# Optimization experiments

Measured on AMD Instinct MI355X. Metric: run time of the kernel, lower is better.

## Reference

```python
import jax, jax.numpy as jnp
import numpy as np

T, B, I, H, O = 1024, 64, 256, 512, 5

def setup_inputs() -> dict:
    key = jax.random.key(0)
    ks = jax.random.split(key, 7)
    s_ih = 1.0 / np.sqrt(H)
    return {
        "inputs": jax.random.normal(ks[0], (T, B, I), dtype=jnp.float32),
        "W_ih": jax.random.uniform(ks[1], (4 * H, I), minval=-s_ih, maxval=s_ih, dtype=jnp.float32),
        "W_hh": jax.random.uniform(ks[2], (4 * H, H), minval=-s_ih, maxval=s_ih, dtype=jnp.float32),
        "b_ih": jax.random.uniform(ks[3], (4 * H,), minval=-s_ih, maxval=s_ih, dtype=jnp.float32),
        "b_hh": jax.random.uniform(ks[4], (4 * H,), minval=-s_ih, maxval=s_ih, dtype=jnp.float32),
        "fc_w": jax.random.uniform(ks[5], (O, H), minval=-s_ih, maxval=s_ih, dtype=jnp.float32),
        "fc_b": jax.random.uniform(ks[6], (O,), minval=-s_ih, maxval=s_ih, dtype=jnp.float32),
    }

def _lstm_step(carry, x_t, W_ih, W_hh, b_ih, b_hh):
    h, c = carry
    # gates: [B, 4H]
    gates = x_t @ W_ih.T + b_ih + h @ W_hh.T + b_hh
    i_g, f_g, g_g, o_g = jnp.split(gates, 4, axis=-1)
    i_g = jax.nn.sigmoid(i_g)
    f_g = jax.nn.sigmoid(f_g)
    g_g = jnp.tanh(g_g)
    o_g = jax.nn.sigmoid(o_g)
    c_new = f_g * c + i_g * g_g
    h_new = o_g * jnp.tanh(c_new)
    return (h_new, c_new), h_new

def reference(inputs, W_ih, W_hh, b_ih, b_hh, fc_w, fc_b):
    batch = inputs.shape[1]
    h0 = jnp.zeros((batch, H), dtype=inputs.dtype)
    c0 = jnp.zeros((batch, H), dtype=inputs.dtype)
    step = lambda carry, x_t: _lstm_step(carry, x_t, W_ih, W_hh, b_ih, b_hh)
    (h_T, c_T), hs = jax.lax.scan(step, (h0, c0), inputs)  # hs: [T, B, H]
    outputs = hs @ fc_w.T + fc_b  # [T, B, O]
    return outputs, (h_T, c_T)
```

## Files before the change

### kernel.cpp

```cpp
#include <hip/hip_runtime.h>
#include <stdint.h>

#define T_ 1024
#define B_ 64
#define I_ 256
#define H_ 512
#define O_ 5
#define NCHAIN 8
#define NB 8
#define JW 16
#define GRID_MAIN 256
#define BLOCK_MAIN 256
#define XBS 264
#define EX_OFF 4096
#define BH (B_*H_)
#define TBO (T_*B_*O_)
#define POISON 0x7F7F7F7Fu

typedef __bf16 bf16x8 __attribute__((ext_vector_type(8)));
typedef float floatx4 __attribute__((ext_vector_type(4)));
typedef unsigned short u16;
typedef unsigned short u16x8 __attribute__((ext_vector_type(8)));
typedef unsigned int u32;
typedef u32 u32x4 __attribute__((ext_vector_type(4)));

__device__ __forceinline__ u16 f2bf(float f) {
  unsigned int u = __float_as_uint(f);
  u += 0x7fffu + ((u >> 16) & 1u);
  return (u16)(u >> 16);
}
__device__ __forceinline__ float bf2f(u16 v) {
  return __uint_as_float(((unsigned int)v) << 16);
}
__device__ __forceinline__ float sigmoid_f(float x) {
  return 1.0f / (1.0f + __expf(-x));
}
__device__ __forceinline__ float tanh_f(float x) {
  return 2.0f / (1.0f + __expf(-2.0f * x)) - 1.0f;
}

__device__ __forceinline__ void store_u32_l3(u32* p, u32 v) {
  asm volatile("global_store_dword %0, %1, off sc0 sc1" :: "v"(p), "v"(v) : "memory");
}

__device__ __forceinline__ void load_h4_l3(const u16* p, u32x4* r) {
  asm volatile(
    "global_load_dwordx4 %0, %4, off sc0 sc1\n\t"
    "global_load_dwordx4 %1, %4, off offset:64 sc0 sc1\n\t"
    "global_load_dwordx4 %2, %4, off offset:128 sc0 sc1\n\t"
    "global_load_dwordx4 %3, %4, off offset:192 sc0 sc1\n\t"
    "s_waitcnt vmcnt(0)"
    : "=&v"(r[0]), "=&v"(r[1]), "=&v"(r[2]), "=&v"(r[3]) : "v"(p) : "memory");
}
__device__ __forceinline__ void load_h6_l3(const u16* p, u32x4* r) {
  asm volatile(
    "global_load_dwordx4 %0, %6, off sc0 sc1\n\t"
    "global_load_dwordx4 %1, %6, off offset:64 sc0 sc1\n\t"
    "global_load_dwordx4 %2, %6, off offset:128 sc0 sc1\n\t"
    "global_load_dwordx4 %3, %6, off offset:192 sc0 sc1\n\t"
    "global_load_dwordx4 %4, %6, off offset:256 sc0 sc1\n\t"
    "global_load_dwordx4 %5, %6, off offset:320 sc0 sc1\n\t"
    "s_waitcnt vmcnt(0)"
    : "=&v"(r[0]), "=&v"(r[1]), "=&v"(r[2]), "=&v"(r[3]), "=&v"(r[4]), "=&v"(r[5])
    : "v"(p) : "memory");
}

__device__ __forceinline__ void barrier_lds() {
  asm volatile("s_waitcnt lgkmcnt(0)\n\ts_barrier" ::: "memory");
}

__device__ __forceinline__ void stage_x(const float* __restrict__ xsrc,
                                        u16 (*xb)[XBS], int u) {
  #pragma unroll
  for (int i = 0; i < 2; ++i) {
    int cid = u + 128 * i;
    int b  = cid >> 5;
    int ko = (cid & 31) * 8;
    const float4* s = (const float4*)(xsrc + (size_t)b * I_ + ko);
    float4 f0 = s[0], f1 = s[1];
    u16x8 uu;
    uu[0]=f2bf(f0.x); uu[1]=f2bf(f0.y); uu[2]=f2bf(f0.z); uu[3]=f2bf(f0.w);
    uu[4]=f2bf(f1.x); uu[5]=f2bf(f1.y); uu[6]=f2bf(f1.z); uu[7]=f2bf(f1.w);
    *(u16x8*)&xb[b][ko] = uu;
  }
}

__global__ __launch_bounds__(BLOCK_MAIN, 1)
void lstm_persistent(const float* __restrict__ x,
                     const float* __restrict__ W_ih,
                     const float* __restrict__ W_hh,
                     const float* __restrict__ b_ih,
                     const float* __restrict__ b_hh,
                     float* __restrict__ out,
                     u16* __restrict__ hist)
{
  __shared__ __align__(16) u16 xbuf[2][NB][XBS];
  __shared__ float part[4 * 4 * 16 * 17];

  const int tid  = threadIdx.x;
  const int wg   = blockIdx.x;
  const int w    = tid >> 6;
  const int lane = tid & 63;
  const int q    = lane >> 4;
  const int n    = lane & 15;
  const int chain = wg & 7;
  const int jslot = wg >> 3;
  const int jbase = jslot * JW;
  const int bbase = chain * NB;

  bf16x8 afrag[4][6];
  #pragma unroll
  for (int g = 0; g < 4; ++g) {
    #pragma unroll
    for (int kk = 0; kk < 6; ++kk) {
      const int kc  = w * 6 + kk;
      const int row = g * H_ + jbase + n;
      const float* src;
      if (kc < 8) src = W_ih + (size_t)row * I_ + kc * 32 + q * 8;
      else        src = W_hh + (size_t)row * H_ + (kc - 8) * 32 + q * 8;
      float4 f0 = ((const float4*)src)[0];
      float4 f1 = ((const float4*)src)[1];
      bf16x8 a;
      a[0]=(__bf16)f0.x; a[1]=(__bf16)f0.y; a[2]=(__bf16)f0.z; a[3]=(__bf16)f0.w;
      a[4]=(__bf16)f1.x; a[5]=(__bf16)f1.y; a[6]=(__bf16)f1.z; a[7]=(__bf16)f1.w;
      afrag[g][kk] = a;
    }
  }

  const int eb = tid >> 4;
  const int ej = tid & 15;
  float bias[4];
  float cval = 0.0f;
  if (tid < 128) {
    #pragma unroll
    for (int g = 0; g < 4; ++g)
      bias[g] = b_ih[g * H_ + jbase + ej] + b_hh[g * H_ + jbase + ej];
  }

  const int nx   = (w == 0) ? 6 : ((w == 1) ? 2 : 0);
  const int hoff = (w == 2) ? 128 : ((w == 3) ? 320 : 0);

  if (tid >= 128) stage_x(x + (size_t)bbase * I_, xbuf[0], tid - 128);
  __syncthreads();

  for (int t = 0; t < T_; ++t) {
    const int sr = t & 1, sw = (t + 1) & 1;

    bf16x8 bfrag[6];
    #pragma unroll
    for (int kk = 0; kk < 6; ++kk)
      if (kk < nx)
        bfrag[kk] = __builtin_bit_cast(bf16x8,
            *(const uint4*)&xbuf[sr][n & 7][(w * 6 + kk) * 32 + q * 8]);

    if (w > 0) {
      const u16* hp = hist + (size_t)t * BH + (size_t)(bbase + (n & 7)) * H_ +
                      hoff + q * 8;
      if (w == 1) {
        u32x4 r[4];
        for (;;) {
          load_h4_l3(hp, r);
          u32 bad = 0;
          #pragma unroll
          for (int i = 0; i < 4; ++i)
            #pragma unroll
            for (int jj = 0; jj < 4; ++jj) bad |= (r[i][jj] == POISON);
          if (!__any((int)bad)) break;
        }
        #pragma unroll
        for (int i = 0; i < 4; ++i)
          bfrag[2 + i] = __builtin_bit_cast(bf16x8, r[i]);
      } else {
        u32x4 r[6];
        for (;;) {
          load_h6_l3(hp, r);
          u32 bad = 0;
          #pragma unroll
          for (int i = 0; i < 6; ++i)
            #pragma unroll
            for (int jj = 0; jj < 4; ++jj) bad |= (r[i][jj] == POISON);
          if (!__any((int)bad)) break;
        }
        #pragma unroll
        for (int i = 0; i < 6; ++i)
          bfrag[i] = __builtin_bit_cast(bf16x8, r[i]);
      }
    }

    floatx4 acc[4] = {};
    #pragma unroll
    for (int kk = 0; kk < 6; ++kk) {
      #pragma unroll
      for (int g = 0; g < 4; ++g)
        acc[g] = __builtin_amdgcn_mfma_f32_16x16x32_bf16(afrag[g][kk], bfrag[kk], acc[g], 0, 0, 0);
    }

    #pragma unroll
    for (int g = 0; g < 4; ++g)
      #pragma unroll
      for (int r = 0; r < 4; ++r)
        part[((w * 4 + g) * 16 + (q * 4 + r)) * 17 + n] = acc[g][r];
    barrier_lds();

    if (tid < 128) {
      float gate[4];
      #pragma unroll
      for (int g = 0; g < 4; ++g) {
        float s = bias[g];
        #pragma unroll
        for (int w2 = 0; w2 < 4; ++w2)
          s += part[((w2 * 4 + g) * 16 + ej) * 17 + eb];
        gate[g] = s;
      }
      const float ig = sigmoid_f(gate[0]);
      const float fg = sigmoid_f(gate[1]);
      const float gg = tanh_f(gate[2]);
      const float og = sigmoid_f(gate[3]);
      cval = fg * cval + ig * gg;
      const float hval = og * tanh_f(cval);
      const int bg = bbase + eb;
      const int jg = jbase + ej;
      const u32 hb = (u32)f2bf(hval);
      const u32 other = __shfl_xor((int)hb, 1, 64);
      if ((tid & 1) == 0) {
        const u32 packed = hb | (other << 16);
        store_u32_l3((u32*)(hist + (size_t)(t + 1) * BH + (size_t)bg * H_ + jg), packed);
      }
      if (t == T_ - 1) {
        out[TBO + (size_t)bg * H_ + jg]      = hval;
        out[TBO + BH + (size_t)bg * H_ + jg] = cval;
      }
    } else {
      const int ts = (t + 1 < T_) ? (t + 1) : (T_ - 1);
      stage_x(x + ((size_t)ts * B_ + bbase) * I_, xbuf[sw], tid - 128);
    }
    barrier_lds();
  }
}

__global__ __launch_bounds__(256)
void fc_kernel(const u16* __restrict__ hist,
               const float* __restrict__ fc_w,
               const float* __restrict__ fc_b,
               float* __restrict__ out)
{
  const int gw   = (blockIdx.x * 256 + threadIdx.x) >> 6;
  const int lane = threadIdx.x & 63;
  const int t = gw >> 6;
  const int b = gw & 63;
  const u16* hrow = hist + ((size_t)(t + 1) * B_ + b) * H_ + lane * 8;
  uint4 hv = *(const uint4*)hrow;
  float h[8];
  {
    u16x8 hu = __builtin_bit_cast(u16x8, hv);
    #pragma unroll
    for (int i = 0; i < 8; ++i) h[i] = bf2f(hu[i]);
  }
  float accs[O_];
  #pragma unroll
  for (int o = 0; o < O_; ++o) {
    const float* wr = fc_w + (size_t)o * H_ + lane * 8;
    float4 w0 = ((const float4*)wr)[0];
    float4 w1 = ((const float4*)wr)[1];
    accs[o] = h[0]*w0.x + h[1]*w0.y + h[2]*w0.z + h[3]*w0.w
            + h[4]*w1.x + h[5]*w1.y + h[6]*w1.z + h[7]*w1.w;
  }
  #pragma unroll
  for (int o = 0; o < O_; ++o)
    #pragma unroll
    for (int off = 32; off > 0; off >>= 1)
      accs[o] += __shfl_down(accs[o], off, 64);
  if (lane == 0) {
    #pragma unroll
    for (int o = 0; o < O_; ++o)
      out[((size_t)t * B_ + b) * O_ + o] = accs[o] + fc_b[o];
  }
}

extern "C" void kernel_launch(void* const* d_in, const int* in_sizes, int n_in,
                              void* d_out, int out_size, void* d_ws, size_t ws_size,
                              hipStream_t stream)
{
  (void)in_sizes; (void)n_in; (void)out_size; (void)ws_size;
  const float* x    = (const float*)d_in[0];
  const float* W_ih = (const float*)d_in[1];
  const float* W_hh = (const float*)d_in[2];
  const float* b_ih = (const float*)d_in[3];
  const float* b_hh = (const float*)d_in[4];
  const float* fc_w = (const float*)d_in[5];
  const float* fc_b = (const float*)d_in[6];
  float* out = (float*)d_out;

  u16* hist = (u16*)((char*)d_ws + EX_OFF);

  hipMemsetAsync(d_ws, 0, EX_OFF + (size_t)BH * 2, stream);
  hipMemsetAsync((char*)d_ws + EX_OFF + (size_t)BH * 2, 0x7F,
                 (size_t)T_ * BH * 2, stream);

  lstm_persistent<<<GRID_MAIN, BLOCK_MAIN, 0, stream>>>(
      x, W_ih, W_hh, b_ih, b_hh, out, hist);
  fc_kernel<<<(T_ * B_) / 4, 256, 0, stream>>>(hist, fc_w, fc_b, out);
}
```

Measured before the change: 2.103 ms.

## Use XCD-local L2 polling for hidden state and drop the trailing barrier

At startup each workgroup reads its XCC id and publishes it, and each chain checks whether all of its workgroups sit on the same XCD. If they do, the h-history polling loads use L2-coherent (sc0) loads instead of system-scope loads, with a periodic fallback to the full-coherence load, and h stores are written both plainly and with sc0 sc1. The partial-sum LDS buffer is double-buffered so the trailing per-step barrier can be removed, and x staging moves to the start of the step. The aim is lower cross-workgroup sync latency per timestep. The risks are stale L2 data if the XCD assumption fails, and LDS hazards from removing the barrier.

Result: slower. 5.434 ms (+158.4%).

```diff
diff --git a/kernel.cpp b/kernel.cpp
--- a/kernel.cpp
+++ b/kernel.cpp
@@ -6,12 +6,12 @@
 #define I_ 256
 #define H_ 512
 #define O_ 5
-#define NCHAIN 8
 #define NB 8
 #define JW 16
 #define GRID_MAIN 256
 #define BLOCK_MAIN 256
 #define XBS 264
+#define PS 18
 #define EX_OFF 4096
 #define BH (B_*H_)
 #define TBO (T_*B_*O_)
@@ -39,8 +39,20 @@
   return 2.0f / (1.0f + __expf(-2.0f * x)) - 1.0f;
 }
 
+__device__ __forceinline__ u32 load_u32_l3(const u32* p) {
+  u32 v;
+  asm volatile("global_load_dword %0, %1, off sc0 sc1\n\ts_waitcnt vmcnt(0)"
+               : "=v"(v) : "v"(p) : "memory");
+  return v;
+}
 __device__ __forceinline__ void store_u32_l3(u32* p, u32 v) {
   asm volatile("global_store_dword %0, %1, off sc0 sc1" :: "v"(p), "v"(v) : "memory");
+}
+__device__ __forceinline__ void store_u32_pub(u32* p, u32 v) {
+  asm volatile(
+    "global_store_dword %0, %1, off\n\t"
+    "global_store_dword %0, %1, off sc0 sc1"
+    :: "v"(p), "v"(v) : "memory");
 }
 
 __device__ __forceinline__ void load_h4_l3(const u16* p, u32x4* r) {
@@ -60,6 +72,27 @@
     "global_load_dwordx4 %3, %6, off offset:192 sc0 sc1\n\t"
     "global_load_dwordx4 %4, %6, off offset:256 sc0 sc1\n\t"
     "global_load_dwordx4 %5, %6, off offset:320 sc0 sc1\n\t"
+    "s_waitcnt vmcnt(0)"
+    : "=&v"(r[0]), "=&v"(r[1]), "=&v"(r[2]), "=&v"(r[3]), "=&v"(r[4]), "=&v"(r[5])
+    : "v"(p) : "memory");
+}
+__device__ __forceinline__ void load_h4_l2(const u16* p, u32x4* r) {
+  asm volatile(
+    "global_load_dwordx4 %0, %4, off sc0\n\t"
+    "global_load_dwordx4 %1, %4, off offset:64 sc0\n\t"
+    "global_load_dwordx4 %2, %4, off offset:128 sc0\n\t"
+    "global_load_dwordx4 %3, %4, off offset:192 sc0\n\t"
+    "s_waitcnt vmcnt(0)"
+    : "=&v"(r[0]), "=&v"(r[1]), "=&v"(r[2]), "=&v"(r[3]) : "v"(p) : "memory");
+}
+__device__ __forceinline__ void load_h6_l2(const u16* p, u32x4* r) {
+  asm volatile(
+    "global_load_dwordx4 %0, %6, off sc0\n\t"
+    "global_load_dwordx4 %1, %6, off offset:64 sc0\n\t"
+    "global_load_dwordx4 %2, %6, off offset:128 sc0\n\t"
+    "global_load_dwordx4 %3, %6, off offset:192 sc0\n\t"
+    "global_load_dwordx4 %4, %6, off offset:256 sc0\n\t"
+    "global_load_dwordx4 %5, %6, off offset:320 sc0\n\t"
     "s_waitcnt vmcnt(0)"
     : "=&v"(r[0]), "=&v"(r[1]), "=&v"(r[2]), "=&v"(r[3]), "=&v"(r[4]), "=&v"(r[5])
     : "v"(p) : "memory");
@@ -92,10 +125,12 @@
                      const float* __restrict__ b_ih,
                      const float* __restrict__ b_hh,
                      float* __restrict__ out,
+                     u32* __restrict__ xslots,
                      u16* __restrict__ hist)
 {
   __shared__ __align__(16) u16 xbuf[2][NB][XBS];
-  __shared__ float part[4 * 4 * 16 * 17];
+  __shared__ float part[2][16 * 16 * PS];
+  __shared__ int s_same;
 
   const int tid  = threadIdx.x;
   const int wg   = blockIdx.x;
@@ -140,11 +175,32 @@
   const int nx   = (w == 0) ? 6 : ((w == 1) ? 2 : 0);
   const int hoff = (w == 2) ? 128 : ((w == 3) ? 320 : 0);
 
+  u32 myxcd;
+  asm volatile("s_getreg_b32 %0, hwreg(HW_REG_XCC_ID)" : "=s"(myxcd));
+  myxcd &= 15u;
+  if (tid == 0) store_u32_l3(&xslots[chain * 32 + jslot], myxcd);
+  if (w == 0) {
+    u32 v = myxcd;
+    if (lane < 32) {
+      const u32* sp = xslots + chain * 32 + lane;
+      do { v = load_u32_l3(sp); } while (v == 0xFFFFFFFFu);
+    }
+    const int ok = __all((int)(v == myxcd));
+    if (tid == 0) s_same = ok;
+  }
+
   if (tid >= 128) stage_x(x + (size_t)bbase * I_, xbuf[0], tid - 128);
   __syncthreads();
+  const bool same_xcd = (s_same != 0);
 
   for (int t = 0; t < T_; ++t) {
-    const int sr = t & 1, sw = (t + 1) & 1;
+    const int pb = t & 1;
+    const int sr = t & 1, sw = sr ^ 1;
+
+    if (w >= 2) {
+      const int ts = (t + 1 < T_) ? (t + 1) : (T_ - 1);
+      stage_x(x + ((size_t)ts * B_ + bbase) * I_, xbuf[sw], tid - 128);
+    }
 
     bf16x8 bfrag[6];
     #pragma unroll
@@ -156,10 +212,13 @@
     if (w > 0) {
       const u16* hp = hist + (size_t)t * BH + (size_t)(bbase + (n & 7)) * H_ +
                       hoff + q * 8;
+      int it = 0;
       if (w == 1) {
         u32x4 r[4];
         for (;;) {
-          load_h4_l3(hp, r);
+          if (same_xcd && ((it & 7) != 7)) load_h4_l2(hp, r);
+          else                             load_h4_l3(hp, r);
+          ++it;
           u32 bad = 0;
           #pragma unroll
           for (int i = 0; i < 4; ++i)
@@ -173,7 +232,9 @@
       } else {
         u32x4 r[6];
         for (;;) {
-          load_h6_l3(hp, r);
+          if (same_xcd && ((it & 7) != 7)) load_h6_l2(hp, r);
+          else                             load_h6_l3(hp, r);
+          ++it;
           u32 bad = 0;
           #pragma unroll
           for (int i = 0; i < 6; ++i)
@@ -199,7 +260,7 @@
     for (int g = 0; g < 4; ++g)
       #pragma unroll
       for (int r = 0; r < 4; ++r)
-        part[((w * 4 + g) * 16 + (q * 4 + r)) * 17 + n] = acc[g][r];
+        part[pb][((w * 4 + g) * 16 + (q * 4 + r)) * PS + n] = acc[g][r];
     barrier_lds();
 
     if (tid < 128) {
@@ -209,7 +270,7 @@
         float s = bias[g];
         #pragma unroll
         for (int w2 = 0; w2 < 4; ++w2)
-          s += part[((w2 * 4 + g) * 16 + ej) * 17 + eb];
+          s += part[pb][((w2 * 4 + g) * 16 + ej) * PS + eb];
         gate[g] = s;
       }
       const float ig = sigmoid_f(gate[0]);
@@ -224,17 +285,13 @@
       const u32 other = __shfl_xor((int)hb, 1, 64);
       if ((tid & 1) == 0) {
         const u32 packed = hb | (other << 16);
-        store_u32_l3((u32*)(hist + (size_t)(t + 1) * BH + (size_t)bg * H_ + jg), packed);
+        store_u32_pub((u32*)(hist + (size_t)(t + 1) * BH + (size_t)bg * H_ + jg), packed);
       }
       if (t == T_ - 1) {
         out[TBO + (size_t)bg * H_ + jg]      = hval;
         out[TBO + BH + (size_t)bg * H_ + jg] = cval;
       }
-    } else {
-      const int ts = (t + 1 < T_) ? (t + 1) : (T_ - 1);
-      stage_x(x + ((size_t)ts * B_ + bbase) * I_, xbuf[sw], tid - 128);
-    }
-    barrier_lds();
+    }
   }
 }
 
@@ -291,13 +348,15 @@
   const float* fc_b = (const float*)d_in[6];
   float* out = (float*)d_out;
 
-  u16* hist = (u16*)((char*)d_ws + EX_OFF);
-
-  hipMemsetAsync(d_ws, 0, EX_OFF + (size_t)BH * 2, stream);
+  u32* xslots = (u32*)d_ws;
+  u16* hist   = (u16*)((char*)d_ws + EX_OFF);
+
+  hipMemsetAsync(d_ws, 0xFF, EX_OFF, stream);
+  hipMemsetAsync((char*)d_ws + EX_OFF, 0, (size_t)BH * 2, stream);
   hipMemsetAsync((char*)d_ws + EX_OFF + (size_t)BH * 2, 0x7F,
                  (size_t)T_ * BH * 2, stream);
 
   lstm_persistent<<<GRID_MAIN, BLOCK_MAIN, 0, stream>>>(
-      x, W_ih, W_hh, b_ih, b_hh, out, hist);
+      x, W_ih, W_hh, b_ih, b_hh, out, xslots, hist);
   fc_kernel<<<(T_ * B_) / 4, 256, 0, stream>>>(hist, fc_w, fc_b, out);
 }
```

## Double-buffer gate partials, drop trailing barrier, and vectorize hidden-state stores

Applied to the files above, without the earlier changes.

The per-step LDS partial-sum buffer is now double-buffered and the x staging moves to the start of each step. Together these let the second workgroup barrier per timestep be removed from the serial recurrence. The bf16 hidden-state publish now gathers eight values per lane group through shuffles and issues one 16-byte system-coherent store instead of several 4-byte stores. Costs are more LDS, extra shuffles, and correctness that depends on the single remaining barrier ordering LDS reuse across steps.

New measurement: 2.314 ms. +10.0%, slower.

```diff
diff --git a/kernel.cpp b/kernel.cpp
--- a/kernel.cpp
+++ b/kernel.cpp
@@ -6,12 +6,12 @@
 #define I_ 256
 #define H_ 512
 #define O_ 5
-#define NCHAIN 8
 #define NB 8
 #define JW 16
 #define GRID_MAIN 256
 #define BLOCK_MAIN 256
 #define XBS 264
+#define PS 18
 #define EX_OFF 4096
 #define BH (B_*H_)
 #define TBO (T_*B_*O_)
@@ -39,8 +39,8 @@
   return 2.0f / (1.0f + __expf(-2.0f * x)) - 1.0f;
 }
 
-__device__ __forceinline__ void store_u32_l3(u32* p, u32 v) {
-  asm volatile("global_store_dword %0, %1, off sc0 sc1" :: "v"(p), "v"(v) : "memory");
+__device__ __forceinline__ void store_u32x4_l3(u32* p, u32x4 v) {
+  asm volatile("global_store_dwordx4 %0, %1, off sc0 sc1" :: "v"(p), "v"(v) : "memory");
 }
 
 __device__ __forceinline__ void load_h4_l3(const u16* p, u32x4* r) {
@@ -95,7 +95,7 @@
                      u16* __restrict__ hist)
 {
   __shared__ __align__(16) u16 xbuf[2][NB][XBS];
-  __shared__ float part[4 * 4 * 16 * 17];
+  __shared__ float part[2][16 * 16 * PS];
 
   const int tid  = threadIdx.x;
   const int wg   = blockIdx.x;
@@ -144,7 +144,13 @@
   __syncthreads();
 
   for (int t = 0; t < T_; ++t) {
-    const int sr = t & 1, sw = (t + 1) & 1;
+    const int pb = t & 1;
+    const int sr = t & 1, sw = sr ^ 1;
+
+    if (w >= 2) {
+      const int ts = (t + 1 < T_) ? (t + 1) : (T_ - 1);
+      stage_x(x + ((size_t)ts * B_ + bbase) * I_, xbuf[sw], tid - 128);
+    }
 
     bf16x8 bfrag[6];
     #pragma unroll
@@ -199,7 +205,7 @@
     for (int g = 0; g < 4; ++g)
       #pragma unroll
       for (int r = 0; r < 4; ++r)
-        part[((w * 4 + g) * 16 + (q * 4 + r)) * 17 + n] = acc[g][r];
+        part[pb][((w * 4 + g) * 16 + (q * 4 + r)) * PS + n] = acc[g][r];
     barrier_lds();
 
     if (tid < 128) {
@@ -209,7 +215,7 @@
         float s = bias[g];
         #pragma unroll
         for (int w2 = 0; w2 < 4; ++w2)
-          s += part[((w2 * 4 + g) * 16 + ej) * 17 + eb];
+          s += part[pb][((w2 * 4 + g) * 16 + ej) * PS + eb];
         gate[g] = s;
       }
       const float ig = sigmoid_f(gate[0]);
@@ -219,22 +225,29 @@
       cval = fg * cval + ig * gg;
       const float hval = og * tanh_f(cval);
       const int bg = bbase + eb;
-      const int jg = jbase + ej;
+
       const u32 hb = (u32)f2bf(hval);
-      const u32 other = __shfl_xor((int)hb, 1, 64);
-      if ((tid & 1) == 0) {
-        const u32 packed = hb | (other << 16);
-        store_u32_l3((u32*)(hist + (size_t)(t + 1) * BH + (size_t)bg * H_ + jg), packed);
+      const u32 ot = (u32)__shfl_xor((int)hb, 1, 64);
+      const u32 lo = (ej & 1) ? ot : hb;
+      const u32 hi = (ej & 1) ? hb : ot;
+      const u32 pk = lo | (hi << 16);
+      const int gl = lane & ~7;
+      const u32 g0 = (u32)__shfl((int)pk, gl + 0, 64);
+      const u32 g1 = (u32)__shfl((int)pk, gl + 2, 64);
+      const u32 g2 = (u32)__shfl((int)pk, gl + 4, 64);
+      const u32 g3 = (u32)__shfl((int)pk, gl + 6, 64);
+      if ((lane & 7) == 0) {
+        u32x4 v4; v4[0] = g0; v4[1] = g1; v4[2] = g2; v4[3] = g3;
+        store_u32x4_l3((u32*)(hist + (size_t)(t + 1) * BH + (size_t)bg * H_ +
+                              jbase + ej),
+                       v4);
       }
       if (t == T_ - 1) {
+        const int jg = jbase + ej;
         out[TBO + (size_t)bg * H_ + jg]      = hval;
         out[TBO + BH + (size_t)bg * H_ + jg] = cval;
       }
-    } else {
-      const int ts = (t + 1 < T_) ? (t + 1) : (T_ - 1);
-      stage_x(x + ((size_t)ts * B_ + bbase) * I_, xbuf[sw], tid - 128);
-    }
-    barrier_lds();
+    }
   }
 }
 
@@ -293,7 +306,7 @@
 
   u16* hist = (u16*)((char*)d_ws + EX_OFF);
 
-  hipMemsetAsync(d_ws, 0, EX_OFF + (size_t)BH * 2, stream);
+  hipMemsetAsync((char*)d_ws + EX_OFF, 0, (size_t)BH * 2, stream);
   hipMemsetAsync((char*)d_ws + EX_OFF + (size_t)BH * 2, 0x7F,
                  (size_t)T_ * BH * 2, stream);
 
```

## Give each wave its own gate rows and share h chunks through LDS

Applied to the files above, without the earlier changes.

Instead of splitting the K dimension across the four waves and reducing partial sums through LDS, each wave now owns 4 hidden columns across all four gates, covering the full K range. Each wave polls one quarter of the h vector from global memory, writes it to LDS and reads the other quarters, so global polling traffic is spread evenly across waves. The gate nonlinearity is computed directly from the MFMA accumulators. The x prefetch is issued by all threads a step ahead and held in registers. The cost is more register pressure from 24 A fragments per wave, idle lanes in the 8-wide batch, and an LDS exchange of h in place of the partial-sum reduction.

After: 3.333 ms. +58.4%, slower.

```diff
diff --git a/kernel.cpp b/kernel.cpp
--- a/kernel.cpp
+++ b/kernel.cpp
@@ -6,12 +6,12 @@
 #define I_ 256
 #define H_ 512
 #define O_ 5
-#define NCHAIN 8
 #define NB 8
 #define JW 16
 #define GRID_MAIN 256
 #define BLOCK_MAIN 256
 #define XBS 264
+#define HSS 40
 #define EX_OFF 4096
 #define BH (B_*H_)
 #define TBO (T_*B_*O_)
@@ -52,37 +52,28 @@
     "s_waitcnt vmcnt(0)"
     : "=&v"(r[0]), "=&v"(r[1]), "=&v"(r[2]), "=&v"(r[3]) : "v"(p) : "memory");
 }
-__device__ __forceinline__ void load_h6_l3(const u16* p, u32x4* r) {
-  asm volatile(
-    "global_load_dwordx4 %0, %6, off sc0 sc1\n\t"
-    "global_load_dwordx4 %1, %6, off offset:64 sc0 sc1\n\t"
-    "global_load_dwordx4 %2, %6, off offset:128 sc0 sc1\n\t"
-    "global_load_dwordx4 %3, %6, off offset:192 sc0 sc1\n\t"
-    "global_load_dwordx4 %4, %6, off offset:256 sc0 sc1\n\t"
-    "global_load_dwordx4 %5, %6, off offset:320 sc0 sc1\n\t"
-    "s_waitcnt vmcnt(0)"
-    : "=&v"(r[0]), "=&v"(r[1]), "=&v"(r[2]), "=&v"(r[3]), "=&v"(r[4]), "=&v"(r[5])
-    : "v"(p) : "memory");
-}
 
 __device__ __forceinline__ void barrier_lds() {
   asm volatile("s_waitcnt lgkmcnt(0)\n\ts_barrier" ::: "memory");
 }
 
-__device__ __forceinline__ void stage_x(const float* __restrict__ xsrc,
-                                        u16 (*xb)[XBS], int u) {
-  #pragma unroll
-  for (int i = 0; i < 2; ++i) {
-    int cid = u + 128 * i;
-    int b  = cid >> 5;
-    int ko = (cid & 31) * 8;
-    const float4* s = (const float4*)(xsrc + (size_t)b * I_ + ko);
-    float4 f0 = s[0], f1 = s[1];
-    u16x8 uu;
-    uu[0]=f2bf(f0.x); uu[1]=f2bf(f0.y); uu[2]=f2bf(f0.z); uu[3]=f2bf(f0.w);
-    uu[4]=f2bf(f1.x); uu[5]=f2bf(f1.y); uu[6]=f2bf(f1.z); uu[7]=f2bf(f1.w);
-    *(u16x8*)&xb[b][ko] = uu;
-  }
+__device__ __forceinline__ void xpf_issue(const float* __restrict__ xsrc,
+                                          int tid, float4* px) {
+  const int b  = tid >> 5;
+  const int ko = (tid & 31) * 8;
+  const float4* s = (const float4*)(xsrc + (size_t)b * I_ + ko);
+  px[0] = s[0];
+  px[1] = s[1];
+}
+__device__ __forceinline__ void xpf_write(u16 (*xb)[XBS], int tid,
+                                          const float4* px) {
+  const int b  = tid >> 5;
+  const int ko = (tid & 31) * 8;
+  const float4 f0 = px[0], f1 = px[1];
+  u16x8 uu;
+  uu[0]=f2bf(f0.x); uu[1]=f2bf(f0.y); uu[2]=f2bf(f0.z); uu[3]=f2bf(f0.w);
+  uu[4]=f2bf(f1.x); uu[5]=f2bf(f1.y); uu[6]=f2bf(f1.z); uu[7]=f2bf(f1.w);
+  *(u16x8*)&xb[b][ko] = uu;
 }
 
 __global__ __launch_bounds__(BLOCK_MAIN, 1)
@@ -95,7 +86,7 @@
                      u16* __restrict__ hist)
 {
   __shared__ __align__(16) u16 xbuf[2][NB][XBS];
-  __shared__ float part[4 * 4 * 16 * 17];
+  __shared__ __align__(16) u16 hshare[16][NB][HSS];
 
   const int tid  = threadIdx.x;
   const int wg   = blockIdx.x;
@@ -107,14 +98,14 @@
   const int jslot = wg >> 3;
   const int jbase = jslot * JW;
   const int bbase = chain * NB;
-
-  bf16x8 afrag[4][6];
-  #pragma unroll
-  for (int g = 0; g < 4; ++g) {
-    #pragma unroll
-    for (int kk = 0; kk < 6; ++kk) {
-      const int kc  = w * 6 + kk;
-      const int row = g * H_ + jbase + n;
+  const int nb   = n & 7;
+  const int jcol = jbase + 4 * w + q;
+
+  bf16x8 afrag[24];
+  {
+    const int row = (n & 3) * H_ + jbase + 4 * w + (n >> 2);
+    #pragma unroll
+    for (int kc = 0; kc < 24; ++kc) {
       const float* src;
       if (kc < 8) src = W_ih + (size_t)row * I_ + kc * 32 + q * 8;
       else        src = W_hh + (size_t)row * H_ + (kc - 8) * 32 + q * 8;
@@ -123,117 +114,98 @@
       bf16x8 a;
       a[0]=(__bf16)f0.x; a[1]=(__bf16)f0.y; a[2]=(__bf16)f0.z; a[3]=(__bf16)f0.w;
       a[4]=(__bf16)f1.x; a[5]=(__bf16)f1.y; a[6]=(__bf16)f1.z; a[7]=(__bf16)f1.w;
-      afrag[g][kk] = a;
-    }
-  }
-
-  const int eb = tid >> 4;
-  const int ej = tid & 15;
+      afrag[kc] = a;
+    }
+  }
+
   float bias[4];
+  #pragma unroll
+  for (int g = 0; g < 4; ++g)
+    bias[g] = b_ih[g * H_ + jcol] + b_hh[g * H_ + jcol];
   float cval = 0.0f;
-  if (tid < 128) {
-    #pragma unroll
-    for (int g = 0; g < 4; ++g)
-      bias[g] = b_ih[g * H_ + jbase + ej] + b_hh[g * H_ + jbase + ej];
-  }
-
-  const int nx   = (w == 0) ? 6 : ((w == 1) ? 2 : 0);
-  const int hoff = (w == 2) ? 128 : ((w == 3) ? 320 : 0);
-
-  if (tid >= 128) stage_x(x + (size_t)bbase * I_, xbuf[0], tid - 128);
+
+  float4 px[2];
+  {
+    xpf_issue(x + (size_t)bbase * I_, tid, px);
+    xpf_write(xbuf[0], tid, px);
+    xpf_issue(x + ((size_t)1 * B_ + bbase) * I_, tid, px);
+  }
   __syncthreads();
 
   for (int t = 0; t < T_; ++t) {
-    const int sr = t & 1, sw = (t + 1) & 1;
-
-    bf16x8 bfrag[6];
-    #pragma unroll
-    for (int kk = 0; kk < 6; ++kk)
-      if (kk < nx)
-        bfrag[kk] = __builtin_bit_cast(bf16x8,
-            *(const uint4*)&xbuf[sr][n & 7][(w * 6 + kk) * 32 + q * 8]);
-
-    if (w > 0) {
-      const u16* hp = hist + (size_t)t * BH + (size_t)(bbase + (n & 7)) * H_ +
-                      hoff + q * 8;
-      if (w == 1) {
-        u32x4 r[4];
-        for (;;) {
-          load_h4_l3(hp, r);
-          u32 bad = 0;
-          #pragma unroll
-          for (int i = 0; i < 4; ++i)
-            #pragma unroll
-            for (int jj = 0; jj < 4; ++jj) bad |= (r[i][jj] == POISON);
-          if (!__any((int)bad)) break;
-        }
+    const int sr = t & 1, sw = sr ^ 1;
+
+    floatx4 acc[4] = {};
+    #pragma unroll
+    for (int kc = 0; kc < 8; ++kc) {
+      bf16x8 xb = __builtin_bit_cast(bf16x8,
+          *(const uint4*)&xbuf[sr][nb][kc * 32 + q * 8]);
+      acc[kc & 3] = __builtin_amdgcn_mfma_f32_16x16x32_bf16(afrag[kc], xb, acc[kc & 3], 0, 0, 0);
+    }
+
+    u32x4 r[4];
+    {
+      const u16* hp = hist + (size_t)t * BH + (size_t)(bbase + nb) * H_ +
+                      w * 128 + q * 8;
+      for (;;) {
+        load_h4_l3(hp, r);
+        u32 bad = 0;
         #pragma unroll
         for (int i = 0; i < 4; ++i)
-          bfrag[2 + i] = __builtin_bit_cast(bf16x8, r[i]);
-      } else {
-        u32x4 r[6];
-        for (;;) {
-          load_h6_l3(hp, r);
-          u32 bad = 0;
           #pragma unroll
-          for (int i = 0; i < 6; ++i)
-            #pragma unroll
-            for (int jj = 0; jj < 4; ++jj) bad |= (r[i][jj] == POISON);
-          if (!__any((int)bad)) break;
-        }
-        #pragma unroll
-        for (int i = 0; i < 6; ++i)
-          bfrag[i] = __builtin_bit_cast(bf16x8, r[i]);
+          for (int jj = 0; jj < 4; ++jj) bad |= (r[i][jj] == POISON);
+        if (!__any((int)bad)) break;
       }
     }
 
-    floatx4 acc[4] = {};
-    #pragma unroll
-    for (int kk = 0; kk < 6; ++kk) {
-      #pragma unroll
-      for (int g = 0; g < 4; ++g)
-        acc[g] = __builtin_amdgcn_mfma_f32_16x16x32_bf16(afrag[g][kk], bfrag[kk], acc[g], 0, 0, 0);
-    }
-
+    #pragma unroll
+    for (int c = 0; c < 4; ++c)
+      if (n < 8)
+        *(u16x8*)&hshare[w * 4 + c][n][q * 8] = __builtin_bit_cast(u16x8, r[c]);
+    #pragma unroll
+    for (int c = 0; c < 4; ++c) {
+      const int kc = 8 + w * 4 + c;
+      acc[kc & 3] = __builtin_amdgcn_mfma_f32_16x16x32_bf16(
+          afrag[kc], __builtin_bit_cast(bf16x8, r[c]), acc[kc & 3], 0, 0, 0);
+    }
+    barrier_lds();
+
+    #pragma unroll
+    for (int hc = 0; hc < 16; ++hc) {
+      if ((hc >> 2) != w) {
+        const int kc = 8 + hc;
+        bf16x8 hb = __builtin_bit_cast(bf16x8,
+            *(const uint4*)&hshare[hc][nb][q * 8]);
+        acc[kc & 3] = __builtin_amdgcn_mfma_f32_16x16x32_bf16(afrag[kc], hb, acc[kc & 3], 0, 0, 0);
+      }
+    }
+
+    float gate[4];
     #pragma unroll
     for (int g = 0; g < 4; ++g)
-      #pragma unroll
-      for (int r = 0; r < 4; ++r)
-        part[((w * 4 + g) * 16 + (q * 4 + r)) * 17 + n] = acc[g][r];
-    barrier_lds();
-
-    if (tid < 128) {
-      float gate[4];
-      #pragma unroll
-      for (int g = 0; g < 4; ++g) {
-        float s = bias[g];
-        #pragma unroll
-        for (int w2 = 0; w2 < 4; ++w2)
-          s += part[((w2 * 4 + g) * 16 + ej) * 17 + eb];
-        gate[g] = s;
-      }
-      const float ig = sigmoid_f(gate[0]);
-      const float fg = sigmoid_f(gate[1]);
-      const float gg = tanh_f(gate[2]);
-      const float og = sigmoid_f(gate[3]);
-      cval = fg * cval + ig * gg;
-      const float hval = og * tanh_f(cval);
-      const int bg = bbase + eb;
-      const int jg = jbase + ej;
-      const u32 hb = (u32)f2bf(hval);
-      const u32 other = __shfl_xor((int)hb, 1, 64);
-      if ((tid & 1) == 0) {
-        const u32 packed = hb | (other << 16);
-        store_u32_l3((u32*)(hist + (size_t)(t + 1) * BH + (size_t)bg * H_ + jg), packed);
-      }
-      if (t == T_ - 1) {
-        out[TBO + (size_t)bg * H_ + jg]      = hval;
-        out[TBO + BH + (size_t)bg * H_ + jg] = cval;
-      }
-    } else {
-      const int ts = (t + 1 < T_) ? (t + 1) : (T_ - 1);
-      stage_x(x + ((size_t)ts * B_ + bbase) * I_, xbuf[sw], tid - 128);
-    }
+      gate[g] = acc[0][g] + acc[1][g] + acc[2][g] + acc[3][g] + bias[g];
+    const float ig = sigmoid_f(gate[0]);
+    const float fg = sigmoid_f(gate[1]);
+    const float gg = tanh_f(gate[2]);
+    const float og = sigmoid_f(gate[3]);
+    cval = fg * cval + ig * gg;
+    const float hval = og * tanh_f(cval);
+
+    const u32 hb32 = (u32)f2bf(hval);
+    const u32 other = (u32)__shfl_xor((int)hb32, 16, 64);
+    if (((q & 1) == 0) && (n < 8)) {
+      const u32 packed = hb32 | (other << 16);
+      store_u32_l3((u32*)(hist + (size_t)(t + 1) * BH +
+                          (size_t)(bbase + n) * H_ + jcol), packed);
+    }
+    if (t == T_ - 1 && n < 8) {
+      out[TBO + (size_t)(bbase + n) * H_ + jcol]      = hval;
+      out[TBO + BH + (size_t)(bbase + n) * H_ + jcol] = cval;
+    }
+
+    xpf_write(xbuf[sw], tid, px);
+    const int ts2 = (t + 2 < T_) ? (t + 2) : (T_ - 1);
+    xpf_issue(x + ((size_t)ts2 * B_ + bbase) * I_, tid, px);
     barrier_lds();
   }
 }
@@ -293,7 +265,7 @@
 
   u16* hist = (u16*)((char*)d_ws + EX_OFF);
 
-  hipMemsetAsync(d_ws, 0, EX_OFF + (size_t)BH * 2, stream);
+  hipMemsetAsync((char*)d_ws + EX_OFF, 0, (size_t)BH * 2, stream);
   hipMemsetAsync((char*)d_ws + EX_OFF + (size_t)BH * 2, 0x7F,
                  (size_t)T_ * BH * 2, stream);
 
```
